# Optimization experiments

Measured on AMD Instinct MI355X. Metric: run time of the kernel, lower is better.

## Reference

```python
import jax, jax.numpy as jnp
import numpy as np

B, S, HID, NH = 4, 2048, 1024, 16
HD = HID // NH  # head_dim = 64


def setup_inputs() -> dict:
    key = jax.random.key(0)
    ks = jax.random.split(key, 5)
    scale = 0.02
    return {
        "hidden_states": jax.random.normal(ks[0], (B, S, HID), dtype=jnp.float32),
        "attention_mask": jnp.zeros((B, 1, 1, S), dtype=jnp.float32),
        "Wq": jax.random.normal(ks[1], (HID, HID), dtype=jnp.float32) * scale,
        "bq": jnp.zeros((HID,), dtype=jnp.float32),
        "Wk": jax.random.normal(ks[2], (HID, HID), dtype=jnp.float32) * scale,
        "bk": jnp.zeros((HID,), dtype=jnp.float32),
        "Wv": jax.random.normal(ks[3], (HID, HID), dtype=jnp.float32) * scale,
        "bv": jnp.zeros((HID,), dtype=jnp.float32),
    }


def _split_heads(x):
    # [B, S, HID] -> [B, NH, S, HD]
    b, s, _ = x.shape
    return x.reshape(b, s, NH, HD).transpose(0, 2, 1, 3)


def reference(hidden_states, attention_mask, Wq, bq, Wk, bk, Wv, bv):
    # Linear projections (torch Linear: x @ W.T + b)
    q = _split_heads(hidden_states @ Wq.T + bq)
    k = _split_heads(hidden_states @ Wk.T + bk)
    v = _split_heads(hidden_states @ Wv.T + bv)

    # scores: [B, NH, S, S]
    scores = jnp.einsum("bhqd,bhkd->bhqk", q, k) / jnp.sqrt(jnp.float32(HD))
    scores = scores + attention_mask  # additive mask, broadcast over heads/query
    weights = jax.nn.softmax(scores, axis=-1)
    # dropout prob = 0 (inference), head_mask = None

    context = jnp.einsum("bhqk,bhkd->bhqd", weights, v)
    # [B, NH, S, HD] -> [B, S, HID]
    context = context.transpose(0, 2, 1, 3).reshape(hidden_states.shape[0], hidden_states.shape[1], HID)
    return context
```

## Files before the change

kernel.cpp:

```cpp
#include <hip/hip_runtime.h>
#include <stdint.h>


typedef float f32x4 __attribute__((ext_vector_type(4)));
typedef float f32x16 __attribute__((ext_vector_type(16)));
typedef __bf16 bf16x4 __attribute__((ext_vector_type(4)));
typedef __bf16 bf16x8 __attribute__((ext_vector_type(8)));
typedef unsigned short ushort_t;
typedef uint32_t u32;

#define MFMA16(a, b, c) __builtin_amdgcn_mfma_f32_16x16x32_bf16(a, b, c, 0, 0, 0)
#define MFMA32(a, b, c) __builtin_amdgcn_mfma_f32_32x32x16_bf16(a, b, c, 0, 0, 0)

__device__ __forceinline__ ushort_t f2b(float f) {
    union { float f; uint32_t u; } x{f};
    uint32_t r = (x.u + 0x7fffu + ((x.u >> 16) & 1u)) >> 16;
    return (ushort_t)r;
}

__device__ __forceinline__ float fexp2(float x) {
#if __has_builtin(__builtin_amdgcn_exp2f)
    return __builtin_amdgcn_exp2f(x);
#else
    return exp2f(x);
#endif
}

__device__ __forceinline__ u32 pkpair(float e, float o) {
    union { float f; u32 u; } xe{e}, xo{o};
    return __builtin_amdgcn_perm(xo.u, xe.u, 0x07060302u);
}

__device__ __forceinline__ bf16x8 mk8(u32 a, u32 b, u32 c, u32 d) {
    union { u32 u[4]; bf16x8 v; } x;
    x.u[0] = a; x.u[1] = b; x.u[2] = c; x.u[3] = d;
    return x.v;
}

__device__ __forceinline__ bf16x8 cat8(bf16x4 a, bf16x4 b) {
    return __builtin_shufflevector(a, b, 0, 1, 2, 3, 4, 5, 6, 7);
}

__device__ __forceinline__ void gld_lds16(const void* g, void* l) {
    __builtin_amdgcn_global_load_lds(
        (const __attribute__((address_space(1))) unsigned int*)g,
        (__attribute__((address_space(3))) unsigned int*)l, 16, 0, 0);
}

__global__ __launch_bounds__(256) void convert_k(
    const float* __restrict__ hs, const float* __restrict__ wq,
    const float* __restrict__ wk, const float* __restrict__ wv,
    ushort_t* __restrict__ hs_b, ushort_t* __restrict__ w_b) {
    size_t c = (size_t)blockIdx.x * 256 + threadIdx.x;
    size_t i = c * 8;
    const size_t NHS = (size_t)8192 * 1024;
    const float* src;
    ushort_t* dst;
    if (i < NHS) { src = hs + i; dst = hs_b + i; }
    else {
        size_t j = i - NHS;
        int w = (int)(j >> 20);
        size_t o = j & ((1u << 20) - 1);
        src = (w == 0 ? wq : (w == 1 ? wk : wv)) + o;
        dst = w_b + ((size_t)w << 20) + o;
    }
    float4 a = *(const float4*)src;
    float4 b = *(const float4*)(src + 4);
    uint32_t p0 = (uint32_t)f2b(a.x) | ((uint32_t)f2b(a.y) << 16);
    uint32_t p1 = (uint32_t)f2b(a.z) | ((uint32_t)f2b(a.w) << 16);
    uint32_t p2 = (uint32_t)f2b(b.x) | ((uint32_t)f2b(b.y) << 16);
    uint32_t p3 = (uint32_t)f2b(b.z) | ((uint32_t)f2b(b.w) << 16);
    uint4 v{p0, p1, p2, p3};
    *(uint4*)dst = v;
}

__global__ __launch_bounds__(256, 2) void qkv_gemm(
    const ushort_t* __restrict__ Ab, const ushort_t* __restrict__ Wb,
    const float* __restrict__ bq, const float* __restrict__ bk,
    const float* __restrict__ bv, ushort_t* __restrict__ q_ws,
    ushort_t* __restrict__ k_ws, ushort_t* __restrict__ vt_ws) {
    __shared__ __align__(16) char smem_raw[65536];
    ushort_t* Ct = (ushort_t*)smem_raw;
    int which = blockIdx.z;
    const ushort_t* W = Wb + ((size_t)which << 20);
    int m0 = blockIdx.x * 128, n0 = blockIdx.y * 128;
    int t = threadIdx.x, lane = t & 63, wave = t >> 6;
    int quad = lane >> 4, l16 = lane & 15;
    int wr = (wave >> 1) * 64, wc = (wave & 1) * 64;
    f32x4 acc[4][4] = {};

    auto stage = [&](int buf, int k0) {
        ushort_t* At = (ushort_t*)smem_raw + buf * 16384;
        ushort_t* Bt = At + 8192;
#pragma unroll
        for (int r = 0; r < 4; r++) {
            int idx = r * 256 + t;
            int row = idx >> 3, ch = idx & 7;
            int sch = (ch ^ (row & 7)) * 8;
            gld_lds16(Ab + (size_t)(m0 + row) * 1024 + k0 + sch, At + idx * 8);
            gld_lds16(W + (size_t)(n0 + row) * 1024 + k0 + sch, Bt + idx * 8);
        }
    };

    stage(0, 0);
    asm volatile("s_waitcnt vmcnt(0)" ::: "memory");
    __syncthreads();
    int cur = 0;

    for (int k0 = 0; k0 < 1024; k0 += 64) {
        if (k0 + 64 < 1024) stage(cur ^ 1, k0 + 64);
        const ushort_t* At = (const ushort_t*)smem_raw + cur * 16384;
        const ushort_t* Bt = At + 8192;
#pragma unroll
        for (int kk = 0; kk < 2; kk++) {
            bf16x8 af[4], bf[4];
#pragma unroll
            for (int i = 0; i < 4; i++) {
                int r = wr + i * 16 + l16;
                af[i] = *(const bf16x8*)(At + r * 64 + ((kk * 4 + quad) ^ (r & 7)) * 8);
            }
#pragma unroll
            for (int j = 0; j < 4; j++) {
                int r = wc + j * 16 + l16;
                bf[j] = *(const bf16x8*)(Bt + r * 64 + ((kk * 4 + quad) ^ (r & 7)) * 8);
            }
#pragma unroll
            for (int i = 0; i < 4; i++)
#pragma unroll
                for (int j = 0; j < 4; j++)
                    acc[i][j] = MFMA16(af[i], bf[j], acc[i][j]);
        }
        asm volatile("s_waitcnt vmcnt(0)" ::: "memory");
        __syncthreads();
        cur ^= 1;
    }

    const float* bias = which == 0 ? bq : (which == 1 ? bk : bv);
    float sc = which == 0 ? (0.125f * 1.44269504f) : 1.0f;
    if (which == 2) {
        for (int j = 0; j < 4; j++) {
            float bias_v = bias[n0 + wc + j * 16 + l16];
            for (int i = 0; i < 4; i++) {
                ushort4 pk;
                pk.x = f2b(acc[i][j].x + bias_v);
                pk.y = f2b(acc[i][j].y + bias_v);
                pk.z = f2b(acc[i][j].z + bias_v);
                pk.w = f2b(acc[i][j].w + bias_v);
                *(ushort4*)(Ct + (wc + j * 16 + l16) * 136 + wr + i * 16 + quad * 4) = pk;
            }
        }
    } else {
        for (int j = 0; j < 4; j++) {
            float bias_v = bias[n0 + wc + j * 16 + l16];
            int col = wc + j * 16 + l16;
            for (int i = 0; i < 4; i++) {
                int rb = wr + i * 16 + quad * 4;
                Ct[(rb + 0) * 136 + col] = f2b((acc[i][j].x + bias_v) * sc);
                Ct[(rb + 1) * 136 + col] = f2b((acc[i][j].y + bias_v) * sc);
                Ct[(rb + 2) * 136 + col] = f2b((acc[i][j].z + bias_v) * sc);
                Ct[(rb + 3) * 136 + col] = f2b((acc[i][j].w + bias_v) * sc);
            }
        }
    }
    __syncthreads();
    for (int r = 0; r < 8; r++) {
        int idx = r * 256 + t;
        int row = idx >> 4, c8 = (idx & 15) * 8;
        uint4 val = *(const uint4*)(Ct + row * 136 + c8);
        if (which == 2) {
            int col = n0 + row, h = col >> 6, d = col & 63;
            int tok = m0 + c8, b = tok >> 11, s = tok & 2047;
            *(uint4*)(vt_ws + ((size_t)(b * 16 + h) * 64 + d) * 2048 + s) = val;
        } else {
            int tok = m0 + row, b = tok >> 11, s = tok & 2047;
            int col = n0 + c8, h = col >> 6, d = col & 63;
            ushort_t* base = which == 0 ? q_ws : k_ws;
            *(uint4*)(base + ((size_t)(b * 16 + h) * 2048 + s) * 64 + d) = val;
        }
    }
}

__global__ __launch_bounds__(256, 2) void attn_k(
    const ushort_t* __restrict__ q_ws, const ushort_t* __restrict__ k_ws,
    const ushort_t* __restrict__ vt_ws, const float* __restrict__ mask,
    float* __restrict__ out) {
    __shared__ __align__(16) char smraw[40960];
    float* Ow = (float*)smraw;
    const float* Mf = (const float*)(smraw + 32768);

    int bh = blockIdx.y, b = bh >> 4, h = bh & 15;
    int q0 = blockIdx.x * 256;
    int t = threadIdx.x, lane = t & 63, w = t >> 6;
    int l31 = lane & 31, hi = lane >> 5;
    const ushort_t* Q = q_ws + (size_t)bh * 2048 * 64;
    const ushort_t* K = k_ws + (size_t)bh * 2048 * 64;
    const ushort_t* Vt = vt_ws + (size_t)bh * 64 * 2048;
    const float* mrow = mask + b * 2048;

    bf16x8 qf[2][4];
#pragma unroll
    for (int qg = 0; qg < 2; qg++)
#pragma unroll
        for (int cs = 0; cs < 4; cs++)
            qf[qg][cs] = *(const bf16x8*)(
                Q + (size_t)(q0 + w * 64 + qg * 32 + l31) * 64 + cs * 16 + hi * 8);
    int co[4];
#pragma unroll
    for (int cs = 0; cs < 4; cs++) co[cs] = ((cs * 2 + hi) ^ (l31 & 7)) * 8;

    f32x16 o00 = {}, o01 = {}, o10 = {}, o11 = {};
    float rs0 = 0.f, rs1 = 0.f;

    auto stage = [&](int buf, int t0) {
        ushort_t* Kb = (ushort_t*)smraw + buf * 8192;
#pragma unroll
        for (int it = 0; it < 2; it++) {
            int idx = it * 256 + t;
            int row = idx >> 3, ch = idx & 7;
            int sch = (ch ^ (row & 7)) * 8;
            gld_lds16(K + (size_t)(t0 + row) * 64 + sch, Kb + idx * 8);
            gld_lds16(Vt + (size_t)row * 2048 + t0 + sch, Kb + 4096 + idx * 8);
        }
    };

    {
        char* Mb = smraw + 32768;
#pragma unroll
        for (int it = 0; it < 2; it++) {
            int idx = it * 256 + t;
            gld_lds16(mrow + idx * 4, Mb + idx * 16);
        }
    }
    stage(0, 0);
    asm volatile("s_waitcnt vmcnt(0)" ::: "memory");
    __syncthreads();
    int cur = 0;

    for (int t0 = 0; t0 < 2048; t0 += 64) {
        if (t0 + 64 < 2048) stage(cur ^ 1, t0 + 64);
        const ushort_t* Kl = (const ushort_t*)smraw + cur * 8192;
        const ushort_t* Vtl = Kl + 4096;

        f32x16 s00 = {}, s01 = {}, s10 = {}, s11 = {};
#pragma unroll
        for (int cs = 0; cs < 4; cs++) {
            bf16x8 k0 = *(const bf16x8*)(Kl + l31 * 64 + co[cs]);
            bf16x8 k1 = *(const bf16x8*)(Kl + (32 + l31) * 64 + co[cs]);
            s00 = MFMA32(k0, qf[0][cs], s00);
            s01 = MFMA32(k1, qf[0][cs], s01);
            s10 = MFMA32(k0, qf[1][cs], s10);
            s11 = MFMA32(k1, qf[1][cs], s11);
        }

        bf16x8 pfr[2][4];
#pragma unroll
        for (int qg = 0; qg < 2; qg++) {
            const f32x16& sa = qg ? s10 : s00;
            const f32x16& sb = qg ? s11 : s01;
            u32 pa[8], pb[8];
            float rst = 0.f;
#pragma unroll
            for (int i = 0; i < 4; i++) {
                float4 bm = *(const float4*)(Mf + t0 + 8 * i + 4 * hi);
                float e0 = fexp2(fmaf(bm.x, 1.44269504f, sa[4 * i + 0]));
                float e1 = fexp2(fmaf(bm.y, 1.44269504f, sa[4 * i + 1]));
                float e2 = fexp2(fmaf(bm.z, 1.44269504f, sa[4 * i + 2]));
                float e3 = fexp2(fmaf(bm.w, 1.44269504f, sa[4 * i + 3]));
                rst += (e0 + e1) + (e2 + e3);
                pa[2 * i] = pkpair(e0, e1);
                pa[2 * i + 1] = pkpair(e2, e3);
            }
#pragma unroll
            for (int i = 0; i < 4; i++) {
                float4 bm = *(const float4*)(Mf + t0 + 32 + 8 * i + 4 * hi);
                float e0 = fexp2(fmaf(bm.x, 1.44269504f, sb[4 * i + 0]));
                float e1 = fexp2(fmaf(bm.y, 1.44269504f, sb[4 * i + 1]));
                float e2 = fexp2(fmaf(bm.z, 1.44269504f, sb[4 * i + 2]));
                float e3 = fexp2(fmaf(bm.w, 1.44269504f, sb[4 * i + 3]));
                rst += (e0 + e1) + (e2 + e3);
                pb[2 * i] = pkpair(e0, e1);
                pb[2 * i + 1] = pkpair(e2, e3);
            }
            if (qg == 0) rs0 += rst; else rs1 += rst;
            pfr[qg][0] = mk8(pa[0], pa[1], pa[2], pa[3]);
            pfr[qg][1] = mk8(pa[4], pa[5], pa[6], pa[7]);
            pfr[qg][2] = mk8(pb[0], pb[1], pb[2], pb[3]);
            pfr[qg][3] = mk8(pb[4], pb[5], pb[6], pb[7]);
        }

#pragma unroll
        for (int cs = 0; cs < 4; cs++) {
            int b0 = ((2 * cs) ^ (l31 & 7)) * 8 + 4 * hi;
            int b1 = ((2 * cs + 1) ^ (l31 & 7)) * 8 + 4 * hi;
            bf16x8 v0 = cat8(*(const bf16x4*)(Vtl + l31 * 64 + b0),
                             *(const bf16x4*)(Vtl + l31 * 64 + b1));
            bf16x8 v1 = cat8(*(const bf16x4*)(Vtl + (32 + l31) * 64 + b0),
                             *(const bf16x4*)(Vtl + (32 + l31) * 64 + b1));
            o00 = MFMA32(v0, pfr[0][cs], o00);
            o01 = MFMA32(v1, pfr[0][cs], o01);
            o10 = MFMA32(v0, pfr[1][cs], o10);
            o11 = MFMA32(v1, pfr[1][cs], o11);
        }

        asm volatile("s_waitcnt vmcnt(0)" ::: "memory");
        __syncthreads();
        cur ^= 1;
    }
    rs0 += __shfl_xor(rs0, 32, 64);
    rs1 += __shfl_xor(rs1, 32, 64);
    float inv0 = 1.f / rs0, inv1 = 1.f / rs1;
#pragma unroll
    for (int qg = 0; qg < 2; qg++) {
        float inv = qg ? inv1 : inv0;
        const f32x16& a0 = qg ? o10 : o00;
        const f32x16& a1 = qg ? o11 : o01;
#pragma unroll
        for (int g = 0; g < 4; g++) {
            f32x4 c0, c1;
#pragma unroll
            for (int r = 0; r < 4; r++) {
                c0[r] = a0[4 * g + r] * inv;
                c1[r] = a1[4 * g + r] * inv;
            }
            *(f32x4*)(Ow + (w * 32 + l31) * 65 + 8 * g + 4 * hi) = c0;
            *(f32x4*)(Ow + (w * 32 + l31) * 65 + 32 + 8 * g + 4 * hi) = c1;
        }
        __syncthreads();
#pragma unroll
        for (int cc = 0; cc < 8; cc++) {
            int c = cc * 256 + t;
            int row = c >> 4, seg = (c & 15) * 4;
            f32x4 vv = *(const f32x4*)(Ow + row * 65 + seg);
            int ql = (row >> 5) * 64 + qg * 32 + (row & 31);
            *(f32x4*)(out + ((size_t)(b * 2048 + q0 + ql)) * 1024 + h * 64 + seg) = vv;
        }
        __syncthreads();
    }
}

extern "C" void kernel_launch(void* const* d_in, const int* in_sizes, int n_in,
                              void* d_out, int out_size, void* d_ws, size_t ws_size,
                              hipStream_t stream) {
    const float* hs = (const float*)d_in[0];
    const float* mask = (const float*)d_in[1];
    const float* wq = (const float*)d_in[2];
    const float* bq = (const float*)d_in[3];
    const float* wk = (const float*)d_in[4];
    const float* bk = (const float*)d_in[5];
    const float* wv = (const float*)d_in[6];
    const float* bv = (const float*)d_in[7];
    float* out = (float*)d_out;
    char* ws = (char*)d_ws;
    ushort_t* hs_b = (ushort_t*)ws;
    ushort_t* w_b = (ushort_t*)(ws + 16777216);
    ushort_t* q_ws = (ushort_t*)(ws + 23068672);
    ushort_t* k_ws = (ushort_t*)(ws + 39845888);
    ushort_t* vt_ws = (ushort_t*)(ws + 56623104);

    convert_k<<<5632, 256, 0, stream>>>(hs, wq, wk, wv, hs_b, w_b);
    qkv_gemm<<<dim3(64, 8, 3), 256, 0, stream>>>(hs_b, w_b, bq, bk, bv, q_ws, k_ws, vt_ws);
    attn_k<<<dim3(8, 64), 256, 0, stream>>>(q_ws, k_ws, vt_ws, mask, out);
}
```

Baseline: 237.3 us.

## Restructure QKV GEMM into 256x128 tiles with 3-stage pipeline and swizzled grid

```diff
diff --git a/kernel.cpp b/kernel.cpp
--- a/kernel.cpp
+++ b/kernel.cpp
@@ -74,109 +74,131 @@
     *(uint4*)dst = v;
 }
 
-__global__ __launch_bounds__(256, 2) void qkv_gemm(
+__global__ __launch_bounds__(512, 4) void qkv_gemm(
     const ushort_t* __restrict__ Ab, const ushort_t* __restrict__ Wb,
     const float* __restrict__ bq, const float* __restrict__ bk,
     const float* __restrict__ bv, ushort_t* __restrict__ q_ws,
     ushort_t* __restrict__ k_ws, ushort_t* __restrict__ vt_ws) {
-    __shared__ __align__(16) char smem_raw[65536];
+    __shared__ __align__(16) char smem_raw[73728];
     ushort_t* Ct = (ushort_t*)smem_raw;
-    int which = blockIdx.z;
+
+    int bid = blockIdx.x;
+    int lid = (bid & 7) * 96 + (bid >> 3);
+    int which = lid >> 8;
+    int rem = lid & 255;
+    int m0 = (rem >> 3) * 256, n0 = (rem & 7) * 128;
     const ushort_t* W = Wb + ((size_t)which << 20);
-    int m0 = blockIdx.x * 128, n0 = blockIdx.y * 128;
+
     int t = threadIdx.x, lane = t & 63, wave = t >> 6;
     int quad = lane >> 4, l16 = lane & 15;
-    int wr = (wave >> 1) * 64, wc = (wave & 1) * 64;
+    int wm = wave >> 1, wn = wave & 1;
+    int wr = wm * 64, wc = wn * 64;
     f32x4 acc[4][4] = {};
 
-    auto stage = [&](int buf, int k0) {
-        ushort_t* At = (ushort_t*)smem_raw + buf * 16384;
+    auto stage = [&](int buf, int k) {
+        int k0 = k * 32;
+        ushort_t* At = (ushort_t*)smem_raw + buf * 12288;
         ushort_t* Bt = At + 8192;
 #pragma unroll
-        for (int r = 0; r < 4; r++) {
-            int idx = r * 256 + t;
-            int row = idx >> 3, ch = idx & 7;
-            int sch = (ch ^ (row & 7)) * 8;
+        for (int r = 0; r < 2; r++) {
+            int idx = r * 512 + t;
+            int row = idx >> 2, ch = idx & 3;
+            int sch = (ch ^ ((row >> 1) & 3)) * 8;
             gld_lds16(Ab + (size_t)(m0 + row) * 1024 + k0 + sch, At + idx * 8);
+        }
+        {
+            int idx = t;
+            int row = idx >> 2, ch = idx & 3;
+            int sch = (ch ^ ((row >> 1) & 3)) * 8;
             gld_lds16(W + (size_t)(n0 + row) * 1024 + k0 + sch, Bt + idx * 8);
         }
     };
 
     stage(0, 0);
-    asm volatile("s_waitcnt vmcnt(0)" ::: "memory");
+    stage(1, 1);
+    int cur = 0;
+
+    for (int s = 0; s < 32; s++) {
+        if (s == 31) asm volatile("s_waitcnt vmcnt(0)" ::: "memory");
+        else         asm volatile("s_waitcnt vmcnt(3)" ::: "memory");
+        __syncthreads();
+        const ushort_t* At = (const ushort_t*)smem_raw + cur * 12288;
+        const ushort_t* Bt = At + 8192;
+        bf16x8 af[4], bf[4];
+#pragma unroll
+        for (int i = 0; i < 4; i++) {
+            int r = wr + i * 16 + l16;
+            af[i] = *(const bf16x8*)(At + r * 32 + ((quad ^ ((r >> 1) & 3)) * 8));
+        }
+#pragma unroll
+        for (int j = 0; j < 4; j++) {
+            int r = wc + j * 16 + l16;
+            bf[j] = *(const bf16x8*)(Bt + r * 32 + ((quad ^ ((r >> 1) & 3)) * 8));
+        }
+#pragma unroll
+        for (int i = 0; i < 4; i++)
+#pragma unroll
+            for (int j = 0; j < 4; j++)
+                acc[i][j] = MFMA16(af[i], bf[j], acc[i][j]);
+        if (s + 2 < 32) stage(cur >= 1 ? cur - 1 : 2, s + 2);
+        cur = cur < 2 ? cur + 1 : 0;
+    }
     __syncthreads();
-    int cur = 0;
-
-    for (int k0 = 0; k0 < 1024; k0 += 64) {
-        if (k0 + 64 < 1024) stage(cur ^ 1, k0 + 64);
-        const ushort_t* At = (const ushort_t*)smem_raw + cur * 16384;
-        const ushort_t* Bt = At + 8192;
-#pragma unroll
-        for (int kk = 0; kk < 2; kk++) {
-            bf16x8 af[4], bf[4];
-#pragma unroll
-            for (int i = 0; i < 4; i++) {
-                int r = wr + i * 16 + l16;
-                af[i] = *(const bf16x8*)(At + r * 64 + ((kk * 4 + quad) ^ (r & 7)) * 8);
-            }
-#pragma unroll
-            for (int j = 0; j < 4; j++) {
-                int r = wc + j * 16 + l16;
-                bf[j] = *(const bf16x8*)(Bt + r * 64 + ((kk * 4 + quad) ^ (r & 7)) * 8);
-            }
-#pragma unroll
-            for (int i = 0; i < 4; i++)
-#pragma unroll
-                for (int j = 0; j < 4; j++)
-                    acc[i][j] = MFMA16(af[i], bf[j], acc[i][j]);
-        }
-        asm volatile("s_waitcnt vmcnt(0)" ::: "memory");
-        __syncthreads();
-        cur ^= 1;
-    }
 
     const float* bias = which == 0 ? bq : (which == 1 ? bk : bv);
     float sc = which == 0 ? (0.125f * 1.44269504f) : 1.0f;
-    if (which == 2) {
-        for (int j = 0; j < 4; j++) {
-            float bias_v = bias[n0 + wc + j * 16 + l16];
-            for (int i = 0; i < 4; i++) {
-                ushort4 pk;
-                pk.x = f2b(acc[i][j].x + bias_v);
-                pk.y = f2b(acc[i][j].y + bias_v);
-                pk.z = f2b(acc[i][j].z + bias_v);
-                pk.w = f2b(acc[i][j].w + bias_v);
-                *(ushort4*)(Ct + (wc + j * 16 + l16) * 136 + wr + i * 16 + quad * 4) = pk;
-            }
-        }
-    } else {
-        for (int j = 0; j < 4; j++) {
-            float bias_v = bias[n0 + wc + j * 16 + l16];
-            int col = wc + j * 16 + l16;
-            for (int i = 0; i < 4; i++) {
-                int rb = wr + i * 16 + quad * 4;
-                Ct[(rb + 0) * 136 + col] = f2b((acc[i][j].x + bias_v) * sc);
-                Ct[(rb + 1) * 136 + col] = f2b((acc[i][j].y + bias_v) * sc);
-                Ct[(rb + 2) * 136 + col] = f2b((acc[i][j].z + bias_v) * sc);
-                Ct[(rb + 3) * 136 + col] = f2b((acc[i][j].w + bias_v) * sc);
-            }
-        }
-    }
-    __syncthreads();
-    for (int r = 0; r < 8; r++) {
-        int idx = r * 256 + t;
-        int row = idx >> 4, c8 = (idx & 15) * 8;
-        uint4 val = *(const uint4*)(Ct + row * 136 + c8);
+#pragma unroll
+    for (int mh = 0; mh < 2; mh++) {
+        bool mine = (wm >> 1) == mh;
+        int mrel = wr - mh * 128;
         if (which == 2) {
-            int col = n0 + row, h = col >> 6, d = col & 63;
-            int tok = m0 + c8, b = tok >> 11, s = tok & 2047;
-            *(uint4*)(vt_ws + ((size_t)(b * 16 + h) * 64 + d) * 2048 + s) = val;
+            if (mine) {
+                for (int j = 0; j < 4; j++) {
+                    float bias_v = bias[n0 + wc + j * 16 + l16];
+                    int nrow = wc + j * 16 + l16;
+                    for (int i = 0; i < 4; i++) {
+                        ushort4 pk;
+                        pk.x = f2b(acc[i][j].x + bias_v);
+                        pk.y = f2b(acc[i][j].y + bias_v);
+                        pk.z = f2b(acc[i][j].z + bias_v);
+                        pk.w = f2b(acc[i][j].w + bias_v);
+                        *(ushort4*)(Ct + nrow * 136 + mrel + i * 16 + quad * 4) = pk;
+                    }
+                }
+            }
         } else {
-            int tok = m0 + row, b = tok >> 11, s = tok & 2047;
-            int col = n0 + c8, h = col >> 6, d = col & 63;
-            ushort_t* base = which == 0 ? q_ws : k_ws;
-            *(uint4*)(base + ((size_t)(b * 16 + h) * 2048 + s) * 64 + d) = val;
-        }
+            if (mine) {
+                for (int j = 0; j < 4; j++) {
+                    float bias_v = bias[n0 + wc + j * 16 + l16];
+                    int col = wc + j * 16 + l16;
+                    for (int i = 0; i < 4; i++) {
+                        int rb = mrel + i * 16 + quad * 4;
+                        Ct[(rb + 0) * 136 + col] = f2b((acc[i][j].x + bias_v) * sc);
+                        Ct[(rb + 1) * 136 + col] = f2b((acc[i][j].y + bias_v) * sc);
+                        Ct[(rb + 2) * 136 + col] = f2b((acc[i][j].z + bias_v) * sc);
+                        Ct[(rb + 3) * 136 + col] = f2b((acc[i][j].w + bias_v) * sc);
+                    }
+                }
+            }
+        }
+        __syncthreads();
+#pragma unroll
+        for (int it = 0; it < 4; it++) {
+            int c = it * 512 + t;
+            int row = c >> 4, c8 = (c & 15) * 8;
+            uint4 val = *(const uint4*)(Ct + row * 136 + c8);
+            if (which == 2) {
+                int col = n0 + row, h = col >> 6, d = col & 63;
+                int tok = m0 + mh * 128 + c8, b = tok >> 11, s = tok & 2047;
+                *(uint4*)(vt_ws + ((size_t)(b * 16 + h) * 64 + d) * 2048 + s) = val;
+            } else {
+                int tok = m0 + mh * 128 + row, b = tok >> 11, s = tok & 2047;
+                int col = n0 + c8, h = col >> 6, d = col & 63;
+                ushort_t* base = which == 0 ? q_ws : k_ws;
+                *(uint4*)(base + ((size_t)(b * 16 + h) * 2048 + s) * 64 + d) = val;
+            }
+        }
+        __syncthreads();
     }
 }
 
@@ -358,6 +380,6 @@
     ushort_t* vt_ws = (ushort_t*)(ws + 56623104);
 
     convert_k<<<5632, 256, 0, stream>>>(hs, wq, wk, wv, hs_b, w_b);
-    qkv_gemm<<<dim3(64, 8, 3), 256, 0, stream>>>(hs_b, w_b, bq, bk, bv, q_ws, k_ws, vt_ws);
+    qkv_gemm<<<768, 512, 0, stream>>>(hs_b, w_b, bq, bk, bv, q_ws, k_ws, vt_ws);
     attn_k<<<dim3(8, 64), 256, 0, stream>>>(q_ws, k_ws, vt_ws, mask, out);
 }
```

Result: slower. 244.5 us (+3.0%).

## Stage 128-key chunks per barrier and raise wave priority around MFMA blocks

Applied to the files above, without the earlier changes.

```diff
diff --git a/kernel.cpp b/kernel.cpp
--- a/kernel.cpp
+++ b/kernel.cpp
@@ -184,9 +184,9 @@
     const ushort_t* __restrict__ q_ws, const ushort_t* __restrict__ k_ws,
     const ushort_t* __restrict__ vt_ws, const float* __restrict__ mask,
     float* __restrict__ out) {
-    __shared__ __align__(16) char smraw[40960];
+    __shared__ __align__(16) char smraw[73728];
     float* Ow = (float*)smraw;
-    const float* Mf = (const float*)(smraw + 32768);
+    const float* Mf = (const float*)(smraw + 65536);
 
     int bh = blockIdx.y, b = bh >> 4, h = bh & 15;
     int q0 = blockIdx.x * 256;
@@ -211,20 +211,23 @@
     f32x16 o00 = {}, o01 = {}, o10 = {}, o11 = {};
     float rs0 = 0.f, rs1 = 0.f;
 
-    auto stage = [&](int buf, int t0) {
-        ushort_t* Kb = (ushort_t*)smraw + buf * 8192;
-#pragma unroll
-        for (int it = 0; it < 2; it++) {
+    auto stage = [&](int buf, int c0) {
+        ushort_t* Bb = (ushort_t*)smraw + buf * 16384;
+#pragma unroll
+        for (int it = 0; it < 4; it++) {
             int idx = it * 256 + t;
-            int row = idx >> 3, ch = idx & 7;
+            int hh = idx >> 9, i9 = idx & 511;
+            int row = i9 >> 3, ch = i9 & 7;
             int sch = (ch ^ (row & 7)) * 8;
-            gld_lds16(K + (size_t)(t0 + row) * 64 + sch, Kb + idx * 8);
-            gld_lds16(Vt + (size_t)row * 2048 + t0 + sch, Kb + 4096 + idx * 8);
+            ushort_t* Kb = Bb + hh * 8192;
+            gld_lds16(K + (size_t)(c0 + hh * 64 + row) * 64 + sch, Kb + i9 * 8);
+            gld_lds16(Vt + (size_t)row * 2048 + c0 + hh * 64 + sch,
+                      Kb + 4096 + i9 * 8);
         }
     };
 
     {
-        char* Mb = smraw + 32768;
+        char* Mb = smraw + 65536;
 #pragma unroll
         for (int it = 0; it < 2; it++) {
             int idx = it * 256 + t;
@@ -236,70 +239,78 @@
     __syncthreads();
     int cur = 0;
 
-    for (int t0 = 0; t0 < 2048; t0 += 64) {
-        if (t0 + 64 < 2048) stage(cur ^ 1, t0 + 64);
-        const ushort_t* Kl = (const ushort_t*)smraw + cur * 8192;
-        const ushort_t* Vtl = Kl + 4096;
-
-        f32x16 s00 = {}, s01 = {}, s10 = {}, s11 = {};
-#pragma unroll
-        for (int cs = 0; cs < 4; cs++) {
-            bf16x8 k0 = *(const bf16x8*)(Kl + l31 * 64 + co[cs]);
-            bf16x8 k1 = *(const bf16x8*)(Kl + (32 + l31) * 64 + co[cs]);
-            s00 = MFMA32(k0, qf[0][cs], s00);
-            s01 = MFMA32(k1, qf[0][cs], s01);
-            s10 = MFMA32(k0, qf[1][cs], s10);
-            s11 = MFMA32(k1, qf[1][cs], s11);
-        }
-
-        bf16x8 pfr[2][4];
-#pragma unroll
-        for (int qg = 0; qg < 2; qg++) {
-            const f32x16& sa = qg ? s10 : s00;
-            const f32x16& sb = qg ? s11 : s01;
-            u32 pa[8], pb[8];
-            float rst = 0.f;
-#pragma unroll
-            for (int i = 0; i < 4; i++) {
-                float4 bm = *(const float4*)(Mf + t0 + 8 * i + 4 * hi);
-                float e0 = fexp2(fmaf(bm.x, 1.44269504f, sa[4 * i + 0]));
-                float e1 = fexp2(fmaf(bm.y, 1.44269504f, sa[4 * i + 1]));
-                float e2 = fexp2(fmaf(bm.z, 1.44269504f, sa[4 * i + 2]));
-                float e3 = fexp2(fmaf(bm.w, 1.44269504f, sa[4 * i + 3]));
-                rst += (e0 + e1) + (e2 + e3);
-                pa[2 * i] = pkpair(e0, e1);
-                pa[2 * i + 1] = pkpair(e2, e3);
-            }
-#pragma unroll
-            for (int i = 0; i < 4; i++) {
-                float4 bm = *(const float4*)(Mf + t0 + 32 + 8 * i + 4 * hi);
-                float e0 = fexp2(fmaf(bm.x, 1.44269504f, sb[4 * i + 0]));
-                float e1 = fexp2(fmaf(bm.y, 1.44269504f, sb[4 * i + 1]));
-                float e2 = fexp2(fmaf(bm.z, 1.44269504f, sb[4 * i + 2]));
-                float e3 = fexp2(fmaf(bm.w, 1.44269504f, sb[4 * i + 3]));
-                rst += (e0 + e1) + (e2 + e3);
-                pb[2 * i] = pkpair(e0, e1);
-                pb[2 * i + 1] = pkpair(e2, e3);
-            }
-            if (qg == 0) rs0 += rst; else rs1 += rst;
-            pfr[qg][0] = mk8(pa[0], pa[1], pa[2], pa[3]);
-            pfr[qg][1] = mk8(pa[4], pa[5], pa[6], pa[7]);
-            pfr[qg][2] = mk8(pb[0], pb[1], pb[2], pb[3]);
-            pfr[qg][3] = mk8(pb[4], pb[5], pb[6], pb[7]);
-        }
-
-#pragma unroll
-        for (int cs = 0; cs < 4; cs++) {
-            int b0 = ((2 * cs) ^ (l31 & 7)) * 8 + 4 * hi;
-            int b1 = ((2 * cs + 1) ^ (l31 & 7)) * 8 + 4 * hi;
-            bf16x8 v0 = cat8(*(const bf16x4*)(Vtl + l31 * 64 + b0),
-                             *(const bf16x4*)(Vtl + l31 * 64 + b1));
-            bf16x8 v1 = cat8(*(const bf16x4*)(Vtl + (32 + l31) * 64 + b0),
-                             *(const bf16x4*)(Vtl + (32 + l31) * 64 + b1));
-            o00 = MFMA32(v0, pfr[0][cs], o00);
-            o01 = MFMA32(v1, pfr[0][cs], o01);
-            o10 = MFMA32(v0, pfr[1][cs], o10);
-            o11 = MFMA32(v1, pfr[1][cs], o11);
+    for (int c0 = 0; c0 < 2048; c0 += 128) {
+        if (c0 + 128 < 2048) stage(cur ^ 1, c0 + 128);
+#pragma unroll
+        for (int hh = 0; hh < 2; hh++) {
+            int t0 = c0 + hh * 64;
+            const ushort_t* Kl = (const ushort_t*)smraw + cur * 16384 + hh * 8192;
+            const ushort_t* Vtl = Kl + 4096;
+
+            f32x16 s00 = {}, s01 = {}, s10 = {}, s11 = {};
+            __builtin_amdgcn_s_setprio(1);
+#pragma unroll
+            for (int cs = 0; cs < 4; cs++) {
+                bf16x8 k0 = *(const bf16x8*)(Kl + l31 * 64 + co[cs]);
+                bf16x8 k1 = *(const bf16x8*)(Kl + (32 + l31) * 64 + co[cs]);
+                s00 = MFMA32(k0, qf[0][cs], s00);
+                s01 = MFMA32(k1, qf[0][cs], s01);
+                s10 = MFMA32(k0, qf[1][cs], s10);
+                s11 = MFMA32(k1, qf[1][cs], s11);
+            }
+            __builtin_amdgcn_s_setprio(0);
+
+            bf16x8 pfr[2][4];
+#pragma unroll
+            for (int qg = 0; qg < 2; qg++) {
+                const f32x16& sa = qg ? s10 : s00;
+                const f32x16& sb = qg ? s11 : s01;
+                u32 pa[8], pb[8];
+                float rst = 0.f;
+#pragma unroll
+                for (int i = 0; i < 4; i++) {
+                    float4 bm = *(const float4*)(Mf + t0 + 8 * i + 4 * hi);
+                    float e0 = fexp2(fmaf(bm.x, 1.44269504f, sa[4 * i + 0]));
+                    float e1 = fexp2(fmaf(bm.y, 1.44269504f, sa[4 * i + 1]));
+                    float e2 = fexp2(fmaf(bm.z, 1.44269504f, sa[4 * i + 2]));
+                    float e3 = fexp2(fmaf(bm.w, 1.44269504f, sa[4 * i + 3]));
+                    rst += (e0 + e1) + (e2 + e3);
+                    pa[2 * i] = pkpair(e0, e1);
+                    pa[2 * i + 1] = pkpair(e2, e3);
+                }
+#pragma unroll
+                for (int i = 0; i < 4; i++) {
+                    float4 bm = *(const float4*)(Mf + t0 + 32 + 8 * i + 4 * hi);
+                    float e0 = fexp2(fmaf(bm.x, 1.44269504f, sb[4 * i + 0]));
+                    float e1 = fexp2(fmaf(bm.y, 1.44269504f, sb[4 * i + 1]));
+                    float e2 = fexp2(fmaf(bm.z, 1.44269504f, sb[4 * i + 2]));
+                    float e3 = fexp2(fmaf(bm.w, 1.44269504f, sb[4 * i + 3]));
+                    rst += (e0 + e1) + (e2 + e3);
+                    pb[2 * i] = pkpair(e0, e1);
+                    pb[2 * i + 1] = pkpair(e2, e3);
+                }
+                if (qg == 0) rs0 += rst; else rs1 += rst;
+                pfr[qg][0] = mk8(pa[0], pa[1], pa[2], pa[3]);
+                pfr[qg][1] = mk8(pa[4], pa[5], pa[6], pa[7]);
+                pfr[qg][2] = mk8(pb[0], pb[1], pb[2], pb[3]);
+                pfr[qg][3] = mk8(pb[4], pb[5], pb[6], pb[7]);
+            }
+
+            __builtin_amdgcn_s_setprio(1);
+#pragma unroll
+            for (int cs = 0; cs < 4; cs++) {
+                int b0 = ((2 * cs) ^ (l31 & 7)) * 8 + 4 * hi;
+                int b1 = ((2 * cs + 1) ^ (l31 & 7)) * 8 + 4 * hi;
+                bf16x8 v0 = cat8(*(const bf16x4*)(Vtl + l31 * 64 + b0),
+                                 *(const bf16x4*)(Vtl + l31 * 64 + b1));
+                bf16x8 v1 = cat8(*(const bf16x4*)(Vtl + (32 + l31) * 64 + b0),
+                                 *(const bf16x4*)(Vtl + (32 + l31) * 64 + b1));
+                o00 = MFMA32(v0, pfr[0][cs], o00);
+                o01 = MFMA32(v1, pfr[0][cs], o01);
+                o10 = MFMA32(v0, pfr[1][cs], o10);
+                o11 = MFMA32(v1, pfr[1][cs], o11);
+            }
+            __builtin_amdgcn_s_setprio(0);
         }
 
         asm volatile("s_waitcnt vmcnt(0)" ::: "memory");
@@ -316,14 +327,14 @@
         const f32x16& a1 = qg ? o11 : o01;
 #pragma unroll
         for (int g = 0; g < 4; g++) {
-            f32x4 c0, c1;
+            f32x4 c0v, c1v;
 #pragma unroll
             for (int r = 0; r < 4; r++) {
-                c0[r] = a0[4 * g + r] * inv;
-                c1[r] = a1[4 * g + r] * inv;
-            }
-            *(f32x4*)(Ow + (w * 32 + l31) * 65 + 8 * g + 4 * hi) = c0;
-            *(f32x4*)(Ow + (w * 32 + l31) * 65 + 32 + 8 * g + 4 * hi) = c1;
+                c0v[r] = a0[4 * g + r] * inv;
+                c1v[r] = a1[4 * g + r] * inv;
+            }
+            *(f32x4*)(Ow + (w * 32 + l31) * 65 + 8 * g + 4 * hi) = c0v;
+            *(f32x4*)(Ow + (w * 32 + l31) * 65 + 32 + 8 * g + 4 * hi) = c1v;
         }
         __syncthreads();
 #pragma unroll
```

Result: slower. 375.5 us (+58.2%).
